# Optimization experiments

Hardware: AMD Instinct MI355X
Metric: run time of the kernel (lower is better)

Reference implementation:

```python
import jax, jax.numpy as jnp
from jax import lax
import numpy as np

B = 8
NUM_ANCHORS = 1047552
PROPOSAL_COUNT = 1000
NMS_THRESHOLD = 0.7
RPN_BBOX_STD_DEV = np.array([0.1, 0.1, 0.2, 0.2], dtype=np.float32)
RPN_NMS_LIMIT = 6000


def setup_inputs() -> dict:
    key = jax.random.key(0)
    k1, k2, k3 = jax.random.split(key, 3)
    rpn_scores = jax.random.uniform(k1, (B, NUM_ANCHORS, 2), dtype=jnp.float32)
    rpn_bbox_delta = jax.random.normal(k2, (B, NUM_ANCHORS, 4), dtype=jnp.float32)
    # Build valid normalized anchors (y1,x1,y2,x2) from uniform randoms.
    u = jax.random.uniform(k3, (NUM_ANCHORS, 4), dtype=jnp.float32)
    cy, cx = u[:, 0], u[:, 1]
    h = u[:, 2] * 0.2 + 0.01
    w = u[:, 3] * 0.2 + 0.01
    anchors = jnp.stack([cy - 0.5 * h, cx - 0.5 * w, cy + 0.5 * h, cx + 0.5 * w], axis=-1)
    anchors = jnp.clip(anchors, 0.0, 1.0)
    return {"rpn_scores": rpn_scores, "rpn_bbox_delta": rpn_bbox_delta, "anchors": anchors}


def _apply_box_deltas(boxes, deltas):
    # boxes: [..., (y1,x1,y2,x2)], deltas: [..., (dy,dx,log(dh),log(dw))]
    h = boxes[..., 2] - boxes[..., 0]
    w = boxes[..., 3] - boxes[..., 1]
    cy = boxes[..., 0] + 0.5 * h + deltas[..., 0] * h
    cx = boxes[..., 1] + 0.5 * w + deltas[..., 1] * w
    h = h * jnp.exp(deltas[..., 2])
    w = w * jnp.exp(deltas[..., 3])
    y1 = cy - 0.5 * h
    x1 = cx - 0.5 * w
    return jnp.stack([y1, x1, y1 + h, x1 + w], axis=-1)


def _nms_indices(boxes):
    # Greedy NMS over boxes already sorted by descending score. boxes: [N,4].
    N = boxes.shape[0]
    areas = (boxes[:, 2] - boxes[:, 0]) * (boxes[:, 3] - boxes[:, 1])

    def body(i, state):
        valid, sel = state
        idx = jnp.argmax(valid)          # first still-valid box = highest score
        has = valid[idx]
        sel = sel.at[i].set(jnp.where(has, idx, -1))
        b = boxes[idx]
        yy1 = jnp.maximum(b[0], boxes[:, 0])
        xx1 = jnp.maximum(b[1], boxes[:, 1])
        yy2 = jnp.minimum(b[2], boxes[:, 2])
        xx2 = jnp.minimum(b[3], boxes[:, 3])
        inter = jnp.maximum(yy2 - yy1, 0.0) * jnp.maximum(xx2 - xx1, 0.0)
        union = areas[idx] + areas - inter
        iou = jnp.where(union > 0, inter / union, 0.0)
        keep = valid & (iou <= NMS_THRESHOLD)
        keep = keep.at[idx].set(False)
        valid = jnp.where(has, keep, valid)
        return valid, sel

    valid0 = jnp.ones((N,), dtype=bool)
    sel0 = jnp.full((PROPOSAL_COUNT,), -1, dtype=jnp.int32)
    _, sel = lax.fori_loop(0, PROPOSAL_COUNT, body, (valid0, sel0))
    return sel


def _nms_single(boxes):
    # boxes: [pre_nms_limit, 4] sorted by score desc -> [proposal_count, 4], zero-padded
    sel = _nms_indices(lax.stop_gradient(boxes))
    props = boxes[jnp.clip(sel, 0)]
    return jnp.where(sel[:, None] >= 0, props, 0.0)


def _forward(rpn_scores, rpn_bbox_delta, anchors):
    scores = rpn_scores[:, :, 1]                                   # [B, A]
    deltas = rpn_bbox_delta * jnp.asarray(RPN_BBOX_STD_DEV)        # [B, A, 4]
    pre_nms_limit = min(RPN_NMS_LIMIT, anchors.shape[0])
    top_scores, ix = lax.top_k(scores, pre_nms_limit)              # [B, pre]
    tgt_deltas = jnp.take_along_axis(deltas, ix[..., None], axis=1)  # [B, pre, 4]
    tgt_anchors = anchors[ix]                                      # [B, pre, 4]
    boxes = _apply_box_deltas(tgt_anchors, tgt_deltas)
    boxes = jnp.clip(boxes, 0.0, 1.0)                              # window (0,0,1,1)
    proposals = jax.vmap(_nms_single)(boxes)                       # [B, proposal_count, 4]
    return proposals


def reference(rpn_scores, rpn_bbox_delta, anchors):
    return _forward(rpn_scores, rpn_bbox_delta, anchors)
```

## Files before the change

### kernel.cpp

```cpp
#include <hip/hip_runtime.h>
#include <stdint.h>

#define NBATCH   8
#define NA       1047552
#define PRE_NMS  6000
#define NPROP    1000
#define BINS     2048
#define HB       64
#define GB       128
#define CAND_CAP 8192
#define NMS_THR  0.7f
#define GBUF     1024
#define SCAP     2048
#define PCHUNK   32
#define PCAP     256
#define REJW     188
#define PTI      64
#define PTJ      256

#define OFF_HIST  ((size_t)0)
#define OFF_BOFF  (OFF_HIST + (size_t)NBATCH*HB*BINS*2)
#define OFF_BCNT  (OFF_BOFF + (size_t)NBATCH*BINS*4)
#define OFF_CTR   (OFF_BCNT + (size_t)NBATCH*BINS*4)
#define CTR_BYTES ((size_t)(32 + NBATCH*PCHUNK*4 + NBATCH*BINS*4))
#define OFF_CAND  (OFF_CTR + 66624)
#define OFF_BOXES (OFF_CAND + (size_t)NBATCH*CAND_CAP*8)
#define OFF_PAIRS (OFF_BOXES + (size_t)NBATCH*PRE_NMS*16)
#define WS_NEEDED (OFF_PAIRS + (size_t)NBATCH*PCHUNK*PCAP*4)

__device__ __forceinline__ unsigned score_bin(float s) {
    int b = (int)(s * (float)BINS);
    if (b < 0) b = 0;
    if (b > BINS - 1) b = BINS - 1;
    return (unsigned)b;
}

__global__ __launch_bounds__(256) void k_hist(const float* __restrict__ scores,
                                              uint16_t* __restrict__ hist) {
    __shared__ uint32_t lh[BINS];
    const int b = blockIdx.y;
    for (int t = threadIdx.x; t < BINS; t += 256) lh[t] = 0;
    __syncthreads();
    const float4* s4 = reinterpret_cast<const float4*>(scores) + (size_t)b * (NA / 2);
    const int n4 = NA / 2;
    const int stride = gridDim.x * 256;
    for (int i = blockIdx.x * 256 + threadIdx.x; i < n4; i += stride) {
        float4 v = s4[i];
        atomicAdd(&lh[score_bin(v.y)], 1u);
        atomicAdd(&lh[score_bin(v.w)], 1u);
    }
    __syncthreads();
    uint16_t* gh = hist + ((size_t)b * HB + blockIdx.x) * BINS;
    for (int t = threadIdx.x; t < BINS; t += 256) gh[t] = (uint16_t)lh[t];
}

__global__ __launch_bounds__(256) void k_thresh(const uint16_t* __restrict__ hist,
                                                uint32_t* __restrict__ boff,
                                                uint32_t* __restrict__ bcnt,
                                                uint32_t* __restrict__ cbin) {
    __shared__ uint32_t hsum[BINS];
    __shared__ uint32_t csum[256];
    __shared__ int sC;
    const int b = blockIdx.x;
    const int t = threadIdx.x;
    if (t == 0) sC = 0;
    const uint32_t* hb32 =
        reinterpret_cast<const uint32_t*>(hist + (size_t)b * HB * BINS);
    for (int p = t; p < BINS / 2; p += 256) {
        uint32_t s0 = 0, s1 = 0;
        for (int k = 0; k < HB; ++k) {
            uint32_t v = hb32[(size_t)k * (BINS / 2) + p];
            s0 += v & 0xffffu;
            s1 += v >> 16;
        }
        hsum[2 * p]     = s0;
        hsum[2 * p + 1] = s1;
    }
    __syncthreads();
    {
        uint32_t c = 0;
        for (int q = 0; q < 8; ++q) c += hsum[t * 8 + q];
        csum[t] = c;
    }
    __syncthreads();
    if (t == 0) {
        uint32_t suf = 0;
        for (int c = 255; c >= 0; --c) { uint32_t v = csum[c]; csum[c] = suf; suf += v; }
    }
    __syncthreads();
    uint32_t acc = csum[t];
    for (int q = 7; q >= 0; --q) {
        int bin = t * 8 + q;
        uint32_t h = hsum[bin];
        boff[(size_t)b * BINS + bin] = acc;
        bcnt[(size_t)b * BINS + bin] = h;
        if (acc + h >= PRE_NMS) atomicMax(&sC, bin);
        acc += h;
    }
    __syncthreads();
    if (t == 0) cbin[b] = (uint32_t)sC;
}

__global__ __launch_bounds__(256) void k_gather(const float* __restrict__ scores,
                                                const uint32_t* __restrict__ cbin,
                                                const uint32_t* __restrict__ boff,
                                                uint32_t* __restrict__ binpos,
                                                uint64_t* __restrict__ cand) {
    __shared__ uint64_t keybuf[GBUF];
    __shared__ uint16_t binbuf[GBUF];
    __shared__ uint32_t bcnts[BINS];
    __shared__ uint32_t gbase[BINS];
    __shared__ uint32_t nbuf;
    const int b = blockIdx.y;
    const unsigned C = cbin[b];
    for (int t = threadIdx.x; t < BINS; t += 256) bcnts[t] = 0;
    if (threadIdx.x == 0) nbuf = 0;
    __syncthreads();
    const float4* s4 = reinterpret_cast<const float4*>(scores) + (size_t)b * (NA / 2);
    const int n4 = NA / 2;
    const int stride = gridDim.x * 256;
    uint64_t* cb = cand + (size_t)b * CAND_CAP;
    for (int i = blockIdx.x * 256 + threadIdx.x; i < n4; i += stride) {
        float4 v = s4[i];
        float sc[2] = { v.y, v.w };
        #pragma unroll
        for (int h = 0; h < 2; ++h) {
            unsigned bin = score_bin(sc[h]);
            if (bin >= C) {
                unsigned idx = 2u * (unsigned)i + (unsigned)h;
                uint64_t key = ((uint64_t)__float_as_uint(sc[h]) << 32) | (uint32_t)(~idx);
                unsigned p = atomicAdd(&nbuf, 1u);
                if (p < GBUF) {
                    keybuf[p] = key; binbuf[p] = (uint16_t)bin;
                    atomicAdd(&bcnts[bin], 1u);
                } else {
                    unsigned pos = boff[(size_t)b * BINS + bin] +
                                   atomicAdd(&binpos[(size_t)b * BINS + bin], 1u);
                    if (pos < CAND_CAP) cb[pos] = key;
                }
            }
        }
    }
    __syncthreads();
    for (int t = threadIdx.x; t < BINS; t += 256) {
        uint32_t c = bcnts[t];
        if (c) gbase[t] = boff[(size_t)b * BINS + t] +
                          atomicAdd(&binpos[(size_t)b * BINS + t], c);
        bcnts[t] = 0;
    }
    __syncthreads();
    unsigned n = nbuf; if (n > GBUF) n = GBUF;
    for (unsigned p = threadIdx.x; p < n; p += 256) {
        unsigned bn = binbuf[p];
        unsigned pos = gbase[bn] + atomicAdd(&bcnts[bn], 1u);
        if (pos < CAND_CAP) cb[pos] = keybuf[p];
    }
}

__global__ __launch_bounds__(256) void k_binsort(const uint32_t* __restrict__ cbin,
                                                 const uint32_t* __restrict__ boff,
                                                 const uint32_t* __restrict__ bcnt,
                                                 uint64_t* __restrict__ cand) {
    __shared__ uint64_t s[SCAP];
    const int b = blockIdx.y;
    const unsigned bin = cbin[b] + blockIdx.x;
    if (bin >= BINS) return;
    unsigned cnt = bcnt[(size_t)b * BINS + bin];
    if (cnt == 0) return;
    unsigned start = boff[(size_t)b * BINS + bin];
    if (start >= CAND_CAP) return;
    if (start + cnt > CAND_CAP) cnt = CAND_CAP - start;
    if (cnt > SCAP) cnt = SCAP;
    unsigned m = 256;
    while (m < cnt) m <<= 1;
    uint64_t* seg = cand + (size_t)b * CAND_CAP + start;
    for (unsigned i = threadIdx.x; i < m; i += 256)
        s[i] = (i < cnt) ? ~seg[i] : ~0ull;
    __syncthreads();
    for (unsigned k = 2; k <= m; k <<= 1) {
        for (unsigned j = k >> 1; j > 0; j >>= 1) {
            for (unsigned i = threadIdx.x; i < m; i += 256) {
                unsigned ixj = i ^ j;
                if (ixj > i) {
                    uint64_t a = s[i], c = s[ixj];
                    bool up = ((i & k) == 0);
                    if ((a > c) == up) { s[i] = c; s[ixj] = a; }
                }
            }
            __syncthreads();
        }
    }
    for (unsigned i = threadIdx.x; i < cnt; i += 256) seg[i] = ~s[i];
}

__global__ __launch_bounds__(256) void k_decode(const uint64_t* __restrict__ cand,
                                                const float* __restrict__ deltas,
                                                const float* __restrict__ anchors,
                                                float4* __restrict__ boxesOut) {
    const int b = blockIdx.y;
    const int r = blockIdx.x * 256 + threadIdx.x;
    if (r >= PRE_NMS) return;
    uint64_t key = cand[(size_t)b * CAND_CAP + r];
    unsigned idx = ~(uint32_t)key;
    float4 o = make_float4(0.f, 0.f, 0.f, 0.f);
    if (idx < NA) {
        float4 a = reinterpret_cast<const float4*>(anchors)[idx];
        float4 d = reinterpret_cast<const float4*>(deltas)[(size_t)b * NA + idx];
        float h = a.z - a.x, w = a.w - a.y;
        float cy = a.x + 0.5f * h + (d.x * 0.1f) * h;
        float cx = a.y + 0.5f * w + (d.y * 0.1f) * w;
        h = h * expf(d.z * 0.2f);
        w = w * expf(d.w * 0.2f);
        float y1 = cy - 0.5f * h, x1 = cx - 0.5f * w;
        float y2 = y1 + h,        x2 = x1 + w;
        o.x = fminf(fmaxf(y1, 0.f), 1.f);
        o.y = fminf(fmaxf(x1, 0.f), 1.f);
        o.z = fminf(fmaxf(y2, 0.f), 1.f);
        o.w = fminf(fmaxf(x2, 0.f), 1.f);
    }
    boxesOut[(size_t)b * PRE_NMS + r] = o;
}

__global__ __launch_bounds__(256) void k_pairs(const float4* __restrict__ boxes,
                                               uint32_t* __restrict__ pcnt,
                                               uint32_t* __restrict__ pairs) {
    const int jb = blockIdx.x;
    const int ib = blockIdx.y;
    const int b  = blockIdx.z;
    const int i0 = ib * PTI;
    const int j0 = jb * PTJ;
    if (i0 > j0 + PTJ - 1) return;
    __shared__ float4 bi[PTI];
    __shared__ float  ai[PTI];
    const int tid = threadIdx.x;
    const float4* bx = boxes + (size_t)b * PRE_NMS;
    if (tid < PTI) {
        int ii = i0 + tid;
        float4 v = (ii < PRE_NMS) ? bx[ii] : make_float4(2.f, 2.f, 2.f, 2.f);
        bi[tid] = v;
        ai[tid] = (v.z - v.x) * (v.w - v.y);
    }
    const int j = j0 + tid;
    float4 vj = (j < PRE_NMS) ? bx[j] : make_float4(2.f, 2.f, 2.f, 2.f);
    const float aj = (vj.z - vj.x) * (vj.w - vj.y);
    __syncthreads();
    uint32_t* pc = pcnt + b * PCHUNK;
    uint32_t* pb = pairs + (size_t)b * PCHUNK * PCAP;
    const bool touchesDiag = (i0 + PTI - 1 >= j0);
    if (touchesDiag) {
        for (int it = 0; it < PTI; ++it) {
            int i = i0 + it;
            if (i >= j) continue;
            float4 vi = bi[it];
            float yy1 = fmaxf(vj.x, vi.x);
            float xx1 = fmaxf(vj.y, vi.y);
            float yy2 = fminf(vj.z, vi.z);
            float xx2 = fminf(vj.w, vi.w);
            float ih = yy2 - yy1, iw = xx2 - xx1;
            float inter = ih * iw;
            float uni = aj + ai[it] - inter;
            if (ih > 0.f && iw > 0.f && inter > NMS_THR * uni) {
                unsigned c = ((unsigned)i + (unsigned)j) & (PCHUNK - 1);
                unsigned pos = atomicAdd(&pc[c], 1u);
                if (pos < PCAP) pb[(size_t)c * PCAP + pos] = ((unsigned)j << 13) | (unsigned)i;
            }
        }
    } else {
        #pragma unroll 4
        for (int it = 0; it < PTI; ++it) {
            float4 vi = bi[it];
            float yy1 = fmaxf(vj.x, vi.x);
            float xx1 = fmaxf(vj.y, vi.y);
            float yy2 = fminf(vj.z, vi.z);
            float xx2 = fminf(vj.w, vi.w);
            float ih = yy2 - yy1, iw = xx2 - xx1;
            float inter = ih * iw;
            float uni = aj + ai[it] - inter;
            if (ih > 0.f && iw > 0.f && inter > NMS_THR * uni) {
                unsigned i = (unsigned)(i0 + it);
                unsigned c = (i + (unsigned)j) & (PCHUNK - 1);
                unsigned pos = atomicAdd(&pc[c], 1u);
                if (pos < PCAP) pb[(size_t)c * PCAP + pos] = ((unsigned)j << 13) | i;
            }
        }
    }
}

__global__ __launch_bounds__(256) void k_nms_emit(const uint32_t* __restrict__ pcnt,
                                                  const uint32_t* __restrict__ pairsIn,
                                                  const float4* __restrict__ boxes,
                                                  float4* __restrict__ out) {
    __shared__ uint32_t sp[PCHUNK * PCAP];
    __shared__ uint32_t cpref[PCHUNK + 1];
    __shared__ uint32_t rejA[REJW], rejB[REJW], pre[REJW + 1];
    __shared__ int changed;
    const int b = blockIdx.x;
    const int tid = threadIdx.x;
    if (tid == 0) {
        unsigned s = 0;
        for (int c = 0; c < PCHUNK; ++c) {
            cpref[c] = s;
            unsigned cc = pcnt[b * PCHUNK + c];
            if (cc > PCAP) cc = PCAP;
            s += cc;
        }
        cpref[PCHUNK] = s;
    }
    for (int t = tid; t < REJW; t += 256) rejA[t] = 0;
    __syncthreads();
    const unsigned np = cpref[PCHUNK];
    for (int c = 0; c < PCHUNK; ++c) {
        unsigned cnt = cpref[c + 1] - cpref[c];
        for (unsigned k = tid; k < cnt; k += 256)
            sp[cpref[c] + k] = pairsIn[((size_t)b * PCHUNK + c) * PCAP + k];
    }
    __syncthreads();
    for (int iter = 0; iter < PRE_NMS; ++iter) {
        for (int t = tid; t < REJW; t += 256) rejB[t] = 0;
        if (tid == 0) changed = 0;
        __syncthreads();
        for (unsigned p = tid; p < np; p += 256) {
            unsigned u = sp[p];
            unsigned j = u >> 13, i = u & 8191u;
            if (!((rejA[i >> 5] >> (i & 31)) & 1u))
                atomicOr(&rejB[j >> 5], 1u << (j & 31));
        }
        __syncthreads();
        for (int t = tid; t < REJW; t += 256) {
            if (rejB[t] != rejA[t]) changed = 1;
            rejA[t] = rejB[t];
        }
        __syncthreads();
        if (!changed) break;
    }
    if (tid == 0) {
        unsigned c2 = 0;
        for (int w = 0; w < REJW; ++w) { pre[w] = c2; c2 += __popc(rejA[w]); }
        pre[REJW] = c2;
    }
    __syncthreads();
    const float4* bx = boxes + (size_t)b * PRE_NMS;
    float4* ob = out + (size_t)b * NPROP;
    for (int j = tid; j < PRE_NMS; j += 256) {
        unsigned w = (unsigned)j >> 5, bit = (unsigned)j & 31;
        if ((rejA[w] >> bit) & 1u) continue;
        unsigned rank = (unsigned)j - (pre[w] + __popc(rejA[w] & ((1u << bit) - 1u)));
        if (rank < NPROP) ob[rank] = bx[j];
    }
}

extern "C" void kernel_launch(void* const* d_in, const int* in_sizes, int n_in,
                              void* d_out, int out_size, void* d_ws, size_t ws_size,
                              hipStream_t stream) {
    const float* scores  = (const float*)d_in[0];
    const float* deltas  = (const float*)d_in[1];
    const float* anchors = (const float*)d_in[2];

    if (ws_size < WS_NEEDED) return;

    char* ws = (char*)d_ws;
    uint16_t* hist   = (uint16_t*)(ws + OFF_HIST);
    uint32_t* boff   = (uint32_t*)(ws + OFF_BOFF);
    uint32_t* bcnt   = (uint32_t*)(ws + OFF_BCNT);
    uint32_t* cbin   = (uint32_t*)(ws + OFF_CTR);
    uint32_t* pcnt   = cbin + NBATCH;
    uint32_t* binpos = pcnt + NBATCH * PCHUNK;
    uint64_t* cand   = (uint64_t*)(ws + OFF_CAND);
    float4*   boxes  = (float4*)(ws + OFF_BOXES);
    uint32_t* pairs  = (uint32_t*)(ws + OFF_PAIRS);

    hipMemsetAsync((void*)cbin, 0, CTR_BYTES, stream);
    hipMemsetAsync(d_out, 0, (size_t)NBATCH * NPROP * 4 * sizeof(float), stream);

    k_hist   <<<dim3(HB, NBATCH), 256, 0, stream>>>(scores, hist);
    k_thresh <<<NBATCH, 256, 0, stream>>>(hist, boff, bcnt, cbin);
    k_gather <<<dim3(GB, NBATCH), 256, 0, stream>>>(scores, cbin, boff, binpos, cand);
    k_binsort<<<dim3(128, NBATCH), 256, 0, stream>>>(cbin, boff, bcnt, cand);
    k_decode <<<dim3((PRE_NMS + 255) / 256, NBATCH), 256, 0, stream>>>(cand, deltas, anchors, boxes);
    k_pairs  <<<dim3((PRE_NMS + PTJ - 1) / PTJ, (PRE_NMS + PTI - 1) / PTI, NBATCH),
               256, 0, stream>>>(boxes, pcnt, pairs);
    k_nms_emit<<<NBATCH, 256, 0, stream>>>(pcnt, pairs, boxes, (float4*)d_out);
}
```

Measured before the change: 431.5 us.

## Parallelize histogram reduction across blocks and register-block the pairwise IoU kernel

The per-batch histogram merge moves out of the single-block threshold kernel into a new wide kernel that sums slices of the per-block histograms and atomically adds them into a zeroed global count array. The threshold kernel then only scans these merged counts. The pair kernel now has each thread handle four j boxes, and the IoU test is rewritten as inter > S*(ai+aj) with S = thr/(1+thr), which removes the union and sign checks. This adds a launch and global atomics, and the reformulated comparison may round differently at the threshold boundary.

```diff
diff --git a/kernel.cpp b/kernel.cpp
--- a/kernel.cpp
+++ b/kernel.cpp
@@ -16,7 +16,9 @@
 #define PCAP     256
 #define REJW     188
 #define PTI      64
-#define PTJ      256
+#define PTJ      1024
+#define JR       4
+#define KS       8
 
 #define OFF_HIST  ((size_t)0)
 #define OFF_BOFF  (OFF_HIST + (size_t)NBATCH*HB*BINS*2)
@@ -54,28 +56,33 @@
     for (int t = threadIdx.x; t < BINS; t += 256) gh[t] = (uint16_t)lh[t];
 }
 
-__global__ __launch_bounds__(256) void k_thresh(const uint16_t* __restrict__ hist,
-                                                uint32_t* __restrict__ boff,
-                                                uint32_t* __restrict__ bcnt,
-                                                uint32_t* __restrict__ cbin) {
+__global__ __launch_bounds__(256) void k_hsum(const uint16_t* __restrict__ hist,
+                                              uint32_t* __restrict__ bcnt) {
+    const int b  = blockIdx.z;
+    const int k0 = blockIdx.y * KS;
+    const unsigned w = blockIdx.x * 256 + threadIdx.x;
+    const uint32_t* hb32 = reinterpret_cast<const uint32_t*>(hist);
+    uint32_t s0 = 0, s1 = 0;
+    #pragma unroll
+    for (int kk = 0; kk < KS; ++kk) {
+        uint32_t v = hb32[((size_t)b * HB + (k0 + kk)) * (BINS / 2) + w];
+        s0 += v & 0xffffu;
+        s1 += v >> 16;
+    }
+    if (s0) atomicAdd(&bcnt[(size_t)b * BINS + 2 * w], s0);
+    if (s1) atomicAdd(&bcnt[(size_t)b * BINS + 2 * w + 1], s1);
+}
+
+__global__ __launch_bounds__(256) void k_thresh2(const uint32_t* __restrict__ bcnt,
+                                                 uint32_t* __restrict__ boff,
+                                                 uint32_t* __restrict__ cbin) {
     __shared__ uint32_t hsum[BINS];
     __shared__ uint32_t csum[256];
     __shared__ int sC;
     const int b = blockIdx.x;
     const int t = threadIdx.x;
     if (t == 0) sC = 0;
-    const uint32_t* hb32 =
-        reinterpret_cast<const uint32_t*>(hist + (size_t)b * HB * BINS);
-    for (int p = t; p < BINS / 2; p += 256) {
-        uint32_t s0 = 0, s1 = 0;
-        for (int k = 0; k < HB; ++k) {
-            uint32_t v = hb32[(size_t)k * (BINS / 2) + p];
-            s0 += v & 0xffffu;
-            s1 += v >> 16;
-        }
-        hsum[2 * p]     = s0;
-        hsum[2 * p + 1] = s1;
-    }
+    for (int p = t; p < BINS; p += 256) hsum[p] = bcnt[(size_t)b * BINS + p];
     __syncthreads();
     {
         uint32_t c = 0;
@@ -93,7 +100,6 @@
         int bin = t * 8 + q;
         uint32_t h = hsum[bin];
         boff[(size_t)b * BINS + bin] = acc;
-        bcnt[(size_t)b * BINS + bin] = h;
         if (acc + h >= PRE_NMS) atomicMax(&sC, bin);
         acc += h;
     }
@@ -234,53 +240,60 @@
     __shared__ float  ai[PTI];
     const int tid = threadIdx.x;
     const float4* bx = boxes + (size_t)b * PRE_NMS;
+    const float S = NMS_THR / (1.0f + NMS_THR);
     if (tid < PTI) {
         int ii = i0 + tid;
         float4 v = (ii < PRE_NMS) ? bx[ii] : make_float4(2.f, 2.f, 2.f, 2.f);
         bi[tid] = v;
-        ai[tid] = (v.z - v.x) * (v.w - v.y);
-    }
-    const int j = j0 + tid;
-    float4 vj = (j < PRE_NMS) ? bx[j] : make_float4(2.f, 2.f, 2.f, 2.f);
-    const float aj = (vj.z - vj.x) * (vj.w - vj.y);
+        ai[tid] = S * ((v.z - v.x) * (v.w - v.y));
+    }
+    float4 vj[JR]; float aj[JR];
+    #pragma unroll
+    for (int r = 0; r < JR; ++r) {
+        int j = j0 + r * 256 + tid;
+        float4 v = (j < PRE_NMS) ? bx[j] : make_float4(2.f, 2.f, 2.f, 2.f);
+        vj[r] = v;
+        aj[r] = S * ((v.z - v.x) * (v.w - v.y));
+    }
     __syncthreads();
     uint32_t* pc = pcnt + b * PCHUNK;
     uint32_t* pb = pairs + (size_t)b * PCHUNK * PCAP;
     const bool touchesDiag = (i0 + PTI - 1 >= j0);
     if (touchesDiag) {
         for (int it = 0; it < PTI; ++it) {
-            int i = i0 + it;
-            if (i >= j) continue;
             float4 vi = bi[it];
-            float yy1 = fmaxf(vj.x, vi.x);
-            float xx1 = fmaxf(vj.y, vi.y);
-            float yy2 = fminf(vj.z, vi.z);
-            float xx2 = fminf(vj.w, vi.w);
-            float ih = yy2 - yy1, iw = xx2 - xx1;
-            float inter = ih * iw;
-            float uni = aj + ai[it] - inter;
-            if (ih > 0.f && iw > 0.f && inter > NMS_THR * uni) {
-                unsigned c = ((unsigned)i + (unsigned)j) & (PCHUNK - 1);
-                unsigned pos = atomicAdd(&pc[c], 1u);
-                if (pos < PCAP) pb[(size_t)c * PCAP + pos] = ((unsigned)j << 13) | (unsigned)i;
+            float air = ai[it];
+            unsigned i = (unsigned)(i0 + it);
+            #pragma unroll
+            for (int r = 0; r < JR; ++r) {
+                float ih = fmaxf(fminf(vj[r].z, vi.z) - fmaxf(vj[r].x, vi.x), 0.f);
+                float iw = fmaxf(fminf(vj[r].w, vi.w) - fmaxf(vj[r].y, vi.y), 0.f);
+                float inter = ih * iw;
+                unsigned j = (unsigned)(j0 + r * 256 + tid);
+                if (inter > air + aj[r] && i < j) {
+                    unsigned c = (i + j) & (PCHUNK - 1);
+                    unsigned pos = atomicAdd(&pc[c], 1u);
+                    if (pos < PCAP) pb[(size_t)c * PCAP + pos] = (j << 13) | i;
+                }
             }
         }
     } else {
-        #pragma unroll 4
+        #pragma unroll 2
         for (int it = 0; it < PTI; ++it) {
             float4 vi = bi[it];
-            float yy1 = fmaxf(vj.x, vi.x);
-            float xx1 = fmaxf(vj.y, vi.y);
-            float yy2 = fminf(vj.z, vi.z);
-            float xx2 = fminf(vj.w, vi.w);
-            float ih = yy2 - yy1, iw = xx2 - xx1;
-            float inter = ih * iw;
-            float uni = aj + ai[it] - inter;
-            if (ih > 0.f && iw > 0.f && inter > NMS_THR * uni) {
-                unsigned i = (unsigned)(i0 + it);
-                unsigned c = (i + (unsigned)j) & (PCHUNK - 1);
-                unsigned pos = atomicAdd(&pc[c], 1u);
-                if (pos < PCAP) pb[(size_t)c * PCAP + pos] = ((unsigned)j << 13) | i;
+            float air = ai[it];
+            #pragma unroll
+            for (int r = 0; r < JR; ++r) {
+                float ih = fmaxf(fminf(vj[r].z, vi.z) - fmaxf(vj[r].x, vi.x), 0.f);
+                float iw = fmaxf(fminf(vj[r].w, vi.w) - fmaxf(vj[r].y, vi.y), 0.f);
+                float inter = ih * iw;
+                if (inter > air + aj[r]) {
+                    unsigned i = (unsigned)(i0 + it);
+                    unsigned j = (unsigned)(j0 + r * 256 + tid);
+                    unsigned c = (i + j) & (PCHUNK - 1);
+                    unsigned pos = atomicAdd(&pc[c], 1u);
+                    if (pos < PCAP) pb[(size_t)c * PCAP + pos] = (j << 13) | i;
+                }
             }
         }
     }
@@ -369,11 +382,12 @@
     float4*   boxes  = (float4*)(ws + OFF_BOXES);
     uint32_t* pairs  = (uint32_t*)(ws + OFF_PAIRS);
 
-    hipMemsetAsync((void*)cbin, 0, CTR_BYTES, stream);
+    hipMemsetAsync((void*)bcnt, 0, (size_t)NBATCH * BINS * 4 + CTR_BYTES, stream);
     hipMemsetAsync(d_out, 0, (size_t)NBATCH * NPROP * 4 * sizeof(float), stream);
 
     k_hist   <<<dim3(HB, NBATCH), 256, 0, stream>>>(scores, hist);
-    k_thresh <<<NBATCH, 256, 0, stream>>>(hist, boff, bcnt, cbin);
+    k_hsum   <<<dim3(BINS / 512, HB / KS, NBATCH), 256, 0, stream>>>(hist, bcnt);
+    k_thresh2<<<NBATCH, 256, 0, stream>>>(bcnt, boff, cbin);
     k_gather <<<dim3(GB, NBATCH), 256, 0, stream>>>(scores, cbin, boff, binpos, cand);
     k_binsort<<<dim3(128, NBATCH), 256, 0, stream>>>(cbin, boff, bcnt, cand);
     k_decode <<<dim3((PRE_NMS + 255) / 256, NBATCH), 256, 0, stream>>>(cand, deltas, anchors, boxes);
```

After: 393.1 us. 8.9% less time.
